# Performance work log

Measured on AMD Instinct MI355X. Metric: run time of the kernel, lower is better.

Reference implementation:

```python
import jax, jax.numpy as jnp
import numpy as np

T, N, DEG = 8, 8192, 15
H = 4


def _gat(x, src, dst, wl, wr, a, b):
    """GATv2Conv with concat=False (heads averaged). x: [N, Cin] -> [N, Cout].
    e_ij = a_h . LeakyReLU(Wl x_j + Wr x_i); softmax over incoming edges of i;
    messages are Wl x_j (PyG GATv2 convention, self-loops already in edge list)."""
    n = x.shape[0]
    h, c = a.shape
    gl = (x @ wl).reshape(n, h, c)  # source-side transform
    gr = (x @ wr).reshape(n, h, c)  # target-side transform
    z = jax.nn.leaky_relu(gl[src] + gr[dst], 0.2)          # [E,H,C]
    e = jnp.einsum('ehc,hc->eh', z, a)                     # [E,H]
    m = jax.ops.segment_max(e, dst, num_segments=n)        # [N,H]
    ex = jnp.exp(e - m[dst])
    den = jax.ops.segment_sum(ex, dst, num_segments=n)     # [N,H]
    msg = jax.ops.segment_sum(ex[:, :, None] * gl[src], dst, num_segments=n)
    return (msg / den[:, :, None]).mean(axis=1) + b


def _d3(x, esrc, edst, wl, wr, a, b):
    # spatio-temporal graph conv: GATv2 applied independently per timestep
    return jax.lax.map(lambda args: _gat(args[0], args[1], args[2], wl, wr, a, b),
                       (x, esrc, edst))


def setup_inputs() -> dict:
    key = jax.random.key(0)
    ks = iter(jax.random.split(key, 32))
    x = jax.random.normal(next(ks), (T, N, 64), dtype=jnp.float32)
    # fixed-degree random graph per timestep + self loops (PyG add_self_loops=True)
    dst_base = jnp.repeat(jnp.arange(N, dtype=jnp.int32), DEG)
    src_r = jax.random.randint(next(ks), (T, N * DEG), 0, N, dtype=jnp.int32)
    loop = jnp.arange(N, dtype=jnp.int32)
    edge_src = jnp.concatenate([src_r, jnp.broadcast_to(loop, (T, N))], axis=1)
    edge_dst = jnp.concatenate([jnp.broadcast_to(dst_base, (T, N * DEG)),
                                jnp.broadcast_to(loop, (T, N))], axis=1)

    def gat_p(k, cin, cout):
        k1, k2, k3 = jax.random.split(k, 3)
        s = 1.0 / np.sqrt(cin)
        return ((jax.random.normal(k1, (cin, H * cout)) * s).astype(jnp.float32),
                (jax.random.normal(k2, (cin, H * cout)) * s).astype(jnp.float32),
                (jax.random.normal(k3, (H, cout)) * s).astype(jnp.float32),
                jnp.zeros((cout,), jnp.float32))

    inp = {"x": x, "edge_src": edge_src, "edge_dst": edge_dst}
    for name, cin, cout in [("c1", 64, 128), ("c2", 128, 64), ("c3", 64, 64), ("c4", 128, 64),
                            ("r11", 64, 64), ("r12", 64, 64), ("r2", 128, 128),
                            ("f11", 64, 64), ("f2", 128, 128)]:
        wl, wr, a, b = gat_p(next(ks), cin, cout)
        inp[name + "_wl"], inp[name + "_wr"], inp[name + "_a"], inp[name + "_b"] = wl, wr, a, b
    # ConvTranspose1d(k=1) == per-node linear conv_ch -> in_channels; then Linear in_channels -> original_dim
    for name, cin, cout in [("r3", 128, 64), ("f3", 128, 64), ("r4", 64, 64), ("f4", 64, 64)]:
        inp[name + "_w"] = (jax.random.normal(next(ks), (cin, cout)) * (1.0 / np.sqrt(cin))).astype(jnp.float32)
        inp[name + "_b"] = jnp.zeros((cout,), jnp.float32)
    return inp


def reference(x, edge_src, edge_dst,
              c1_wl, c1_wr, c1_a, c1_b, c2_wl, c2_wr, c2_a, c2_b,
              c3_wl, c3_wr, c3_a, c3_b, c4_wl, c4_wr, c4_a, c4_b,
              r11_wl, r11_wr, r11_a, r11_b, r12_wl, r12_wr, r12_a, r12_b,
              r2_wl, r2_wr, r2_a, r2_b, r3_w, r3_b, r4_w, r4_b,
              f11_wl, f11_wr, f11_a, f11_b, f2_wl, f2_wr, f2_a, f2_b,
              f3_w, f3_b, f4_w, f4_b):
    elu = jax.nn.elu
    out = elu(_d3(x, edge_src, edge_dst, c1_wl, c1_wr, c1_a, c1_b))           # [T,N,128]
    emb = elu(_d3(out, edge_src, edge_dst, c2_wl, c2_wr, c2_a, c2_b))         # [T,N,64]
    emb = elu(jnp.concatenate([_d3(emb, edge_src, edge_dst, c3_wl, c3_wr, c3_a, c3_b), emb], -1))  # [T,N,128]
    emb = elu(_d3(emb, edge_src, edge_dst, c4_wl, c4_wr, c4_a, c4_b))         # [T,N,64]

    # reconstruction branch on edges at t = -1
    s1, d1 = edge_src[-1], edge_dst[-1]
    r = elu(_gat(emb[-1], s1, d1, r11_wl, r11_wr, r11_a, r11_b))
    r = elu(jnp.concatenate([_gat(r, s1, d1, r12_wl, r12_wr, r12_a, r12_b), r], -1))  # [N,128]
    # F.dropout in eval mode -> identity
    r = elu(_gat(r, s1, d1, r2_wl, r2_wr, r2_a, r2_b))
    r = jnp.tanh(r @ r3_w + r3_b)
    recon = r @ r4_w + r4_b

    # forecasting branch on edges at t = -2 (original reuses reconstruct12 here)
    s2, d2 = edge_src[-2], edge_dst[-2]
    f = elu(_gat(emb[-2], s2, d2, f11_wl, f11_wr, f11_a, f11_b))
    f = elu(jnp.concatenate([_gat(f, s2, d2, r12_wl, r12_wr, r12_a, r12_b), f], -1))
    f = elu(_gat(f, s2, d2, f2_wl, f2_wr, f2_a, f2_b))
    f = jnp.tanh(f @ f3_w + f3_b)
    forecast = f @ f4_w + f4_b
    return (recon, forecast, emb)
```

## Files before the change

### kernel.cpp

```cpp
#include <hip/hip_runtime.h>
#include <cmath>

constexpr int T_   = 8;
constexpr int N_   = 8192;
constexpr int DEG_ = 15;
constexpr int E_   = N_ * (DEG_ + 1);
constexpr float L2E_ = 1.44269504f;

__device__ __forceinline__ float elu1(float v) {
  return v > 0.f ? v : exp2f(v * L2E_) - 1.f;
}

typedef __attribute__((ext_vector_type(8))) short bf16x8;
typedef __attribute__((ext_vector_type(4))) float f32x4;

__device__ __forceinline__ ushort f2bf(float x) {
  uint u = __float_as_uint(x);
  return (ushort)((u + 0x7FFFu + ((u >> 16) & 1u)) >> 16);
}
__device__ __forceinline__ float bf2f(ushort h) {
  return __uint_as_float(((uint)h) << 16);
}

template<int CTRL>
__device__ __forceinline__ float dpp_add(float x) {
  const int t = __builtin_amdgcn_mov_dpp(__float_as_int(x), CTRL, 0xf, 0xf, true);
  return x + __int_as_float(t);
}
__device__ __forceinline__ float row_reduce16(float x) {
  x = dpp_add<0x121>(x);
  x = dpp_add<0x122>(x);
  x = dpp_add<0x124>(x);
  x = dpp_add<0x128>(x);
  return x;
}

__global__ __launch_bounds__(256) void pad_edges(
    const int* __restrict__ es, uint* __restrict__ es16, int total)
{
  const int idx = blockIdx.x * 256 + threadIdx.x;
  if (idx >= total) return;
  const int t = idx >> 13, i = idx & (N_ - 1);
  const int* e = es + (size_t)t * E_ + (size_t)i * DEG_;
  uint o[16];
  #pragma unroll
  for (int k = 0; k < DEG_; k++) o[k] = (uint)e[k];
  o[15] = (uint)i;
  uint4* dst = (uint4*)(es16 + (size_t)idx * 16);
  dst[0] = make_uint4(o[0], o[1], o[2], o[3]);
  dst[1] = make_uint4(o[4], o[5], o[6], o[7]);
  dst[2] = make_uint4(o[8], o[9], o[10], o[11]);
  dst[3] = make_uint4(o[12], o[13], o[14], o[15]);
}

__global__ __launch_bounds__(256) void split_x(
    const float* __restrict__ X, ushort* __restrict__ XH, ushort* __restrict__ XL, int n4)
{
  const int i = blockIdx.x * 256 + threadIdx.x;
  if (i >= n4) return;
  const float4 v = ((const float4*)X)[i];
  const ushort h0 = f2bf(v.x), h1 = f2bf(v.y), h2 = f2bf(v.z), h3 = f2bf(v.w);
  ushort4 hh; hh.x = h0; hh.y = h1; hh.z = h2; hh.w = h3;
  ushort4 ll;
  ll.x = f2bf(v.x - bf2f(h0)); ll.y = f2bf(v.y - bf2f(h1));
  ll.z = f2bf(v.z - bf2f(h2)); ll.w = f2bf(v.w - bf2f(h3));
  ((ushort4*)XH)[i] = hh;
  ((ushort4*)XL)[i] = ll;
}

struct WTable {
  const float* wl[9]; const float* wr[9];
  int lgK[9]; int lgHC[9]; int off[9];
};
__global__ __launch_bounds__(256) void split_wt_all(
    WTable tb, ushort* __restrict__ WH, ushort* __restrict__ WL)
{
  const int y = blockIdx.y;
  const int lgK = tb.lgK[y], lgHC = tb.lgHC[y];
  const int n2 = 2 << (lgK + lgHC);
  const int idx = blockIdx.x * 256 + threadIdx.x;
  if (idx >= n2) return;
  const int k = idx & ((1 << lgK) - 1);
  const int n = (idx >> lgK) & ((1 << lgHC) - 1);
  const int s = idx >> (lgK + lgHC);
  const float* W = s ? tb.wr[y] : tb.wl[y];
  const float v = W[((size_t)k << lgHC) + n];
  const ushort h = f2bf(v);
  WH[tb.off[y] + idx] = h;
  WL[tb.off[y] + idx] = f2bf(v - bf2f(h));
}

__global__ __launch_bounds__(256) void gemm_mfma(
    const ushort* __restrict__ Ah, const ushort* __restrict__ Al,
    const ushort* __restrict__ Wh, const ushort* __restrict__ Wl,
    float* __restrict__ Cl, float* __restrict__ Cr,
    int M, int Ncol, int K, int nt)
{
  __shared__ alignas(16) ushort lAh[4 * 1032];
  __shared__ alignas(16) ushort lAl[4 * 1032];
  __shared__ alignas(16) ushort lBh[4 * 520];
  __shared__ alignas(16) ushort lBl[4 * 520];

  const int z = blockIdx.z;
  const int t = (z < nt) ? z : z - nt;
  const int side = (z < nt) ? 0 : 1;
  const ushort* __restrict__ Bh = Wh + (size_t)side * Ncol * K;
  const ushort* __restrict__ Bl = Wl + (size_t)side * Ncol * K;
  float* __restrict__ C = (side ? Cr : Cl) + (size_t)t * M * Ncol;
  const size_t aoff = (size_t)t * M * K;

  const int bm = blockIdx.x * 128, bn = blockIdx.y * 64;
  const int tid = threadIdx.x;
  const int wid = tid >> 6, lane = tid & 63;
  const int l15 = lane & 15, lk = lane >> 4;

  f32x4 acc[2][4] = {};

  for (int k0 = 0; k0 < K; k0 += 32) {
    #pragma unroll
    for (int c = 0; c < 2; c++) {
      const int ch = tid + c * 256;
      const int row = ch >> 2, kc = ch & 3;
      const size_t ga = aoff + (size_t)(bm + row) * K + (k0 + kc * 8);
      *(uint4*)&lAh[kc * 1032 + row * 8] = *(const uint4*)(Ah + ga);
      *(uint4*)&lAl[kc * 1032 + row * 8] = *(const uint4*)(Al + ga);
    }
    {
      const int col = tid >> 2, kc = tid & 3;
      const size_t gb = (size_t)(bn + col) * K + (k0 + kc * 8);
      *(uint4*)&lBh[kc * 520 + col * 8] = *(const uint4*)(Bh + gb);
      *(uint4*)&lBl[kc * 520 + col * 8] = *(const uint4*)(Bl + gb);
    }
    __syncthreads();

    bf16x8 ah[2], al[2], bh4[4], bl4[4];
    const int r0 = wid * 32;
    #pragma unroll
    for (int rf = 0; rf < 2; rf++) {
      const int ro = (r0 + rf * 16 + l15) * 8;
      ah[rf] = *(const bf16x8*)&lAh[lk * 1032 + ro];
      al[rf] = *(const bf16x8*)&lAl[lk * 1032 + ro];
    }
    #pragma unroll
    for (int cf = 0; cf < 4; cf++) {
      const int co = (cf * 16 + l15) * 8;
      bh4[cf] = *(const bf16x8*)&lBh[lk * 520 + co];
      bl4[cf] = *(const bf16x8*)&lBl[lk * 520 + co];
    }
    #pragma unroll
    for (int rf = 0; rf < 2; rf++)
      #pragma unroll
      for (int cf = 0; cf < 4; cf++) {
        acc[rf][cf] = __builtin_amdgcn_mfma_f32_16x16x32_bf16(ah[rf], bh4[cf], acc[rf][cf], 0, 0, 0);
        acc[rf][cf] = __builtin_amdgcn_mfma_f32_16x16x32_bf16(ah[rf], bl4[cf], acc[rf][cf], 0, 0, 0);
        acc[rf][cf] = __builtin_amdgcn_mfma_f32_16x16x32_bf16(al[rf], bh4[cf], acc[rf][cf], 0, 0, 0);
      }
    __syncthreads();
  }

  #pragma unroll
  for (int rf = 0; rf < 2; rf++)
    #pragma unroll
    for (int cf = 0; cf < 4; cf++) {
      const int col = bn + cf * 16 + l15;
      #pragma unroll
      for (int reg = 0; reg < 4; reg++) {
        const int row = bm + wid * 32 + rf * 16 + lk * 4 + reg;
        C[(size_t)row * Ncol + col] = acc[rf][cf][reg];
      }
    }
}

template<int EPI>
__global__ __launch_bounds__(256) void gemm_k(
    const float* __restrict__ A, const float* __restrict__ B,
    float* __restrict__ C, const float* __restrict__ bias,
    int M, int Ncol, int K)
{
  __shared__ float As[16][68];
  __shared__ float Bs[16][64];

  const int tid = threadIdx.x;
  const int tx = tid & 15, ty = tid >> 4;
  const int bm = blockIdx.x * 64, bn = blockIdx.y * 64;

  const int arow = tid >> 2;
  const int akc  = (tid & 3) * 4;
  const int brow = tid >> 4;
  const int bc4  = (tid & 15) * 4;

  float acc[4][4];
  #pragma unroll
  for (int i = 0; i < 4; i++)
    #pragma unroll
    for (int j = 0; j < 4; j++) acc[i][j] = 0.f;

  for (int k0 = 0; k0 < K; k0 += 16) {
    const float4 va = *(const float4*)(A + (size_t)(bm + arow) * K + (k0 + akc));
    const float4 vb = *(const float4*)(B + (size_t)(k0 + brow) * Ncol + (bn + bc4));
    As[akc + 0][arow] = va.x; As[akc + 1][arow] = va.y;
    As[akc + 2][arow] = va.z; As[akc + 3][arow] = va.w;
    *(float4*)&Bs[brow][bc4] = vb;
    __syncthreads();
    #pragma unroll
    for (int kk = 0; kk < 16; kk++) {
      const float4 av = *(const float4*)&As[kk][ty * 4];
      const float4 bv = *(const float4*)&Bs[kk][tx * 4];
      const float a4[4] = {av.x, av.y, av.z, av.w};
      const float b4[4] = {bv.x, bv.y, bv.z, bv.w};
      #pragma unroll
      for (int i = 0; i < 4; i++)
        #pragma unroll
        for (int j = 0; j < 4; j++)
          acc[i][j] = fmaf(a4[i], b4[j], acc[i][j]);
    }
    __syncthreads();
  }

  #pragma unroll
  for (int i = 0; i < 4; i++) {
    const int row = bm + ty * 4 + i;
    const int col = bn + tx * 4;
    float v[4] = {acc[i][0], acc[i][1], acc[i][2], acc[i][3]};
    #pragma unroll
    for (int j = 0; j < 4; j++) v[j] += bias[col + j];
    if (EPI == 1) {
      #pragma unroll
      for (int j = 0; j < 4; j++) v[j] = tanhf(v[j]);
    }
    *(float4*)(C + (size_t)row * Ncol + col) = make_float4(v[0], v[1], v[2], v[3]);
  }
}

template<bool CONCAT, bool WF32>
__global__ __launch_bounds__(256) void gat_agg256(
    const float* __restrict__ GL, const float* __restrict__ GR,
    const float* __restrict__ aw_, const float* __restrict__ bias,
    const uint* __restrict__ es16, float* __restrict__ out,
    const float* __restrict__ csrc,
    ushort* __restrict__ SHo, ushort* __restrict__ SLo)
{
  constexpr int C = 64;
  constexpr int OSTR = CONCAT ? 128 : 64;

  const int lane = threadIdx.x & 63;
  const int wid  = threadIdx.x >> 6;
  const int t    = blockIdx.x >> 11;
  const int gid  = blockIdx.x * 4 + wid;

  const float* __restrict__ gl = GL + (size_t)t * N_ * 256;
  const uint*  __restrict__ ep = es16 + (size_t)gid * 16;
  const uint lo16 = (uint)lane << 4;

  float gr[4], a6[4], a4c[4];
  {
    const float4 gv = *(const float4*)(GR + (size_t)gid * 256 + lane * 4);
    const float4 av = *(const float4*)(aw_ + lane * 4);
    gr[0] = gv.x; gr[1] = gv.y; gr[2] = gv.z; gr[3] = gv.w;
    a6[0] = 0.6f * L2E_ * av.x; a6[1] = 0.6f * L2E_ * av.y;
    a6[2] = 0.6f * L2E_ * av.z; a6[3] = 0.6f * L2E_ * av.w;
    a4c[0] = 0.4f * L2E_ * av.x; a4c[1] = 0.4f * L2E_ * av.y;
    a4c[2] = 0.4f * L2E_ * av.z; a4c[3] = 0.4f * L2E_ * av.w;
  }

  float acc[4] = {0.f, 0.f, 0.f, 0.f};
  float den = 0.f, m = 0.f;

  #pragma unroll
  for (int b = 0; b < 4; b++) {
    const uint4 j4 = *(const uint4*)(ep + b * 4);
    uint off[4];
    off[0] = (j4.x << 10) + lo16;
    off[1] = (j4.y << 10) + lo16;
    off[2] = (j4.z << 10) + lo16;
    off[3] = (j4.w << 10) + lo16;
    float g[4][4];
    #pragma unroll
    for (int q = 0; q < 4; q++) {
      const float4 v = *(const float4*)((const char*)gl + off[q]);
      g[q][0] = v.x; g[q][1] = v.y; g[q][2] = v.z; g[q][3] = v.w;
    }
    float p[4];
    #pragma unroll
    for (int q = 0; q < 4; q++) {
      float s = 0.f;
      #pragma unroll
      for (int u = 0; u < 4; u++) {
        const float z = g[q][u] + gr[u];
        s = fmaf(z, a6[u], s);
        s = fmaf(fabsf(z), a4c[u], s);
      }
      p[q] = s;
    }
    #pragma unroll
    for (int q = 0; q < 4; q++) p[q] = row_reduce16(p[q]);

    const float bmax = fmaxf(fmaxf(p[0], p[1]), fmaxf(p[2], p[3]));
    if (b == 0) {
      m = bmax;
    } else {
      const float nm = fmaxf(m, bmax);
      const float sc = exp2f(m - nm);
      den *= sc;
      #pragma unroll
      for (int u = 0; u < 4; u++) acc[u] *= sc;
      m = nm;
    }
    #pragma unroll
    for (int q = 0; q < 4; q++) {
      const float w = exp2f(p[q] - m);
      den += w;
      #pragma unroll
      for (int u = 0; u < 4; u++) acc[u] = fmaf(w, g[q][u], acc[u]);
    }
  }

  const float inv = 0.25f / den;
  #pragma unroll
  for (int u = 0; u < 4; u++) acc[u] *= inv;
  #pragma unroll
  for (int u = 0; u < 4; u++) {
    acc[u] += __shfl_xor(acc[u], 16);
    acc[u] += __shfl_xor(acc[u], 32);
  }

  if (lane < 16) {
    float o[4];
    #pragma unroll
    for (int u = 0; u < 4; u++)
      o[u] = elu1(acc[u] + bias[lane * 4 + u]);
    if (WF32)
      *(float4*)(out + (size_t)gid * OSTR + lane * 4) = make_float4(o[0], o[1], o[2], o[3]);
    ushort4 hh, ll;
    hh.x = f2bf(o[0]); hh.y = f2bf(o[1]); hh.z = f2bf(o[2]); hh.w = f2bf(o[3]);
    ll.x = f2bf(o[0] - bf2f(hh.x)); ll.y = f2bf(o[1] - bf2f(hh.y));
    ll.z = f2bf(o[2] - bf2f(hh.z)); ll.w = f2bf(o[3] - bf2f(hh.w));
    *(ushort4*)(SHo + (size_t)gid * OSTR + lane * 4) = hh;
    *(ushort4*)(SLo + (size_t)gid * OSTR + lane * 4) = ll;
  } else if (CONCAT && lane < 32) {
    const int q = lane - 16;
    const float4 v = *(const float4*)(csrc + (size_t)gid * C + q * 4);
    const float o0 = elu1(v.x), o1 = elu1(v.y), o2 = elu1(v.z), o3 = elu1(v.w);
    if (WF32)
      *(float4*)(out + (size_t)gid * OSTR + C + q * 4) = make_float4(o0, o1, o2, o3);
    ushort4 hh, ll;
    hh.x = f2bf(o0); hh.y = f2bf(o1); hh.z = f2bf(o2); hh.w = f2bf(o3);
    ll.x = f2bf(o0 - bf2f(hh.x)); ll.y = f2bf(o1 - bf2f(hh.y));
    ll.z = f2bf(o2 - bf2f(hh.z)); ll.w = f2bf(o3 - bf2f(hh.w));
    *(ushort4*)(SHo + (size_t)gid * OSTR + C + q * 4) = hh;
    *(ushort4*)(SLo + (size_t)gid * OSTR + C + q * 4) = ll;
  }
}

template<bool WF32, bool SPLIT>
__global__ __launch_bounds__(256) void gat_agg512(
    const float* __restrict__ GL, const float* __restrict__ GR,
    const float* __restrict__ aw_, const float* __restrict__ bias,
    const uint* __restrict__ es16, float* __restrict__ out,
    ushort* __restrict__ SHo, ushort* __restrict__ SLo)
{
  const int lane = threadIdx.x & 63;
  const int wid  = threadIdx.x >> 6;
  const int t    = blockIdx.x >> 11;
  const int gid  = blockIdx.x * 4 + wid;

  const float* __restrict__ gl = GL + (size_t)t * N_ * 512;
  const uint*  __restrict__ ep = es16 + (size_t)gid * 16;

  const int s  = lane & 15;
  const int cb = ((lane >> 4) << 7) + (s << 3);
  const uint laneoff = (uint)cb << 2;

  float gr[8], a6[8], a4[8];
  {
    const float4 g0 = *(const float4*)(GR + (size_t)gid * 512 + cb);
    const float4 g1 = *(const float4*)(GR + (size_t)gid * 512 + cb + 4);
    const float4 a0 = *(const float4*)(aw_ + cb);
    const float4 a1 = *(const float4*)(aw_ + cb + 4);
    gr[0] = g0.x; gr[1] = g0.y; gr[2] = g0.z; gr[3] = g0.w;
    gr[4] = g1.x; gr[5] = g1.y; gr[6] = g1.z; gr[7] = g1.w;
    a6[0] = 0.6f * L2E_ * a0.x; a6[1] = 0.6f * L2E_ * a0.y;
    a6[2] = 0.6f * L2E_ * a0.z; a6[3] = 0.6f * L2E_ * a0.w;
    a6[4] = 0.6f * L2E_ * a1.x; a6[5] = 0.6f * L2E_ * a1.y;
    a6[6] = 0.6f * L2E_ * a1.z; a6[7] = 0.6f * L2E_ * a1.w;
    a4[0] = 0.4f * L2E_ * a0.x; a4[1] = 0.4f * L2E_ * a0.y;
    a4[2] = 0.4f * L2E_ * a0.z; a4[3] = 0.4f * L2E_ * a0.w;
    a4[4] = 0.4f * L2E_ * a1.x; a4[5] = 0.4f * L2E_ * a1.y;
    a4[6] = 0.4f * L2E_ * a1.z; a4[7] = 0.4f * L2E_ * a1.w;
  }

  float acc[8] = {0.f, 0.f, 0.f, 0.f, 0.f, 0.f, 0.f, 0.f};
  float den = 0.f, m = 0.f;

  #pragma unroll
  for (int b = 0; b < 4; b++) {
    const uint4 j4 = *(const uint4*)(ep + b * 4);
    uint off[4];
    off[0] = (j4.x << 11) + laneoff;
    off[1] = (j4.y << 11) + laneoff;
    off[2] = (j4.z << 11) + laneoff;
    off[3] = (j4.w << 11) + laneoff;
    float g[4][8];
    #pragma unroll
    for (int q = 0; q < 4; q++) {
      const float4 v0 = *(const float4*)((const char*)gl + off[q]);
      const float4 v1 = *(const float4*)((const char*)gl + off[q] + 16);
      g[q][0] = v0.x; g[q][1] = v0.y; g[q][2] = v0.z; g[q][3] = v0.w;
      g[q][4] = v1.x; g[q][5] = v1.y; g[q][6] = v1.z; g[q][7] = v1.w;
    }
    float p[4];
    #pragma unroll
    for (int q = 0; q < 4; q++) {
      float sc = 0.f;
      #pragma unroll
      for (int u = 0; u < 8; u++) {
        const float z = g[q][u] + gr[u];
        sc = fmaf(z, a6[u], sc);
        sc = fmaf(fabsf(z), a4[u], sc);
      }
      p[q] = sc;
    }
    #pragma unroll
    for (int q = 0; q < 4; q++) p[q] = row_reduce16(p[q]);

    const float bmax = fmaxf(fmaxf(p[0], p[1]), fmaxf(p[2], p[3]));
    if (b == 0) {
      m = bmax;
    } else {
      const float nm = fmaxf(m, bmax);
      const float sc = exp2f(m - nm);
      den *= sc;
      #pragma unroll
      for (int u = 0; u < 8; u++) acc[u] *= sc;
      m = nm;
    }
    #pragma unroll
    for (int q = 0; q < 4; q++) {
      const float w = exp2f(p[q] - m);
      den += w;
      #pragma unroll
      for (int u = 0; u < 8; u++) acc[u] = fmaf(w, g[q][u], acc[u]);
    }
  }

  const float inv = 0.25f / den;
  #pragma unroll
  for (int u = 0; u < 8; u++) acc[u] *= inv;
  #pragma unroll
  for (int u = 0; u < 8; u++) {
    acc[u] += __shfl_xor(acc[u], 16);
    acc[u] += __shfl_xor(acc[u], 32);
  }

  if (lane < 16) {
    float o[8];
    #pragma unroll
    for (int u = 0; u < 8; u++)
      o[u] = elu1(acc[u] + bias[s * 8 + u]);
    if (WF32) {
      *(float4*)(out + (size_t)gid * 128 + s * 8)     = make_float4(o[0], o[1], o[2], o[3]);
      *(float4*)(out + (size_t)gid * 128 + s * 8 + 4) = make_float4(o[4], o[5], o[6], o[7]);
    }
    if (SPLIT) {
      ushort4 h0, h1, l0, l1;
      h0.x = f2bf(o[0]); h0.y = f2bf(o[1]); h0.z = f2bf(o[2]); h0.w = f2bf(o[3]);
      h1.x = f2bf(o[4]); h1.y = f2bf(o[5]); h1.z = f2bf(o[6]); h1.w = f2bf(o[7]);
      l0.x = f2bf(o[0] - bf2f(h0.x)); l0.y = f2bf(o[1] - bf2f(h0.y));
      l0.z = f2bf(o[2] - bf2f(h0.z)); l0.w = f2bf(o[3] - bf2f(h0.w));
      l1.x = f2bf(o[4] - bf2f(h1.x)); l1.y = f2bf(o[5] - bf2f(h1.y));
      l1.z = f2bf(o[6] - bf2f(h1.z)); l1.w = f2bf(o[7] - bf2f(h1.w));
      *(ushort4*)(SHo + (size_t)gid * 128 + s * 8)     = h0;
      *(ushort4*)(SHo + (size_t)gid * 128 + s * 8 + 4) = h1;
      *(ushort4*)(SLo + (size_t)gid * 128 + s * 8)     = l0;
      *(ushort4*)(SLo + (size_t)gid * 128 + s * 8 + 4) = l1;
    }
  }
}

extern "C" void kernel_launch(void* const* d_in, const int* in_sizes, int n_in,
                              void* d_out, int out_size, void* d_ws, size_t ws_size,
                              hipStream_t stream)
{
  (void)in_sizes; (void)n_in; (void)out_size; (void)ws_size;

  const float* x  = (const float*)d_in[0];
  const int*   es = (const int*)d_in[1];
  const float *c1_wl=(const float*)d_in[3], *c1_wr=(const float*)d_in[4], *c1_a=(const float*)d_in[5], *c1_b=(const float*)d_in[6];
  const float *c2_wl=(const float*)d_in[7], *c2_wr=(const float*)d_in[8], *c2_a=(const float*)d_in[9], *c2_b=(const float*)d_in[10];
  const float *c3_wl=(const float*)d_in[11],*c3_wr=(const float*)d_in[12],*c3_a=(const float*)d_in[13],*c3_b=(const float*)d_in[14];
  const float *c4_wl=(const float*)d_in[15],*c4_wr=(const float*)d_in[16],*c4_a=(const float*)d_in[17],*c4_b=(const float*)d_in[18];
  const float *r11_wl=(const float*)d_in[19],*r11_wr=(const float*)d_in[20],*r11_a=(const float*)d_in[21],*r11_b=(const float*)d_in[22];
  const float *r12_wl=(const float*)d_in[23],*r12_wr=(const float*)d_in[24],*r12_a=(const float*)d_in[25],*r12_b=(const float*)d_in[26];
  const float *r2_wl=(const float*)d_in[27],*r2_wr=(const float*)d_in[28],*r2_a=(const float*)d_in[29],*r2_b=(const float*)d_in[30];
  const float *f11_wl=(const float*)d_in[31],*f11_wr=(const float*)d_in[32],*f11_a=(const float*)d_in[33],*f11_b=(const float*)d_in[34];
  const float *f2_wl=(const float*)d_in[35],*f2_wr=(const float*)d_in[36],*f2_a=(const float*)d_in[37],*f2_b=(const float*)d_in[38];
  const float *r3_w=(const float*)d_in[39], *r3_b=(const float*)d_in[40];
  const float *f3_w=(const float*)d_in[41], *f3_b=(const float*)d_in[42];
  const float *r4_w=(const float*)d_in[43], *r4_b=(const float*)d_in[44];
  const float *f4_w=(const float*)d_in[45], *f4_b=(const float*)d_in[46];

  float* ws = (float*)d_ws;
  float* GL = ws;
  float* GR = GL + (size_t)16777216;
  float* A1 = GR + (size_t)16777216;
  float* B0 = A1 + (size_t)T_ * N_ * 64;
  float* B1 = B0 + (size_t)N_ * 128;
  ushort* SH  = (ushort*)(B1 + (size_t)N_ * 128);
  ushort* SL  = SH + (size_t)8388608;
  ushort* SH2 = SL + (size_t)8388608;
  ushort* SL2 = SH2 + (size_t)8388608;
  ushort* WH  = SL2 + (size_t)8388608;
  ushort* WL  = WH + (size_t)589824;
  uint*  ES16 = (uint*)(WL + (size_t)589824);

  float* recon = (float*)d_out;
  float* fcst  = recon + (size_t)N_ * 64;
  float* emb   = fcst + (size_t)N_ * 64;

  const dim3 blk(256);

  pad_edges<<<dim3(T_ * N_ / 256), blk, 0, stream>>>(es, ES16, T_ * N_);
  split_x<<<dim3(T_ * N_ * 64 / 4 / 256), blk, 0, stream>>>(x, SH, SL, T_ * N_ * 64 / 4);
  WTable tb;
  const float* wls[9] = {c1_wl, c2_wl, c3_wl, c4_wl, r11_wl, r12_wl, r2_wl, f11_wl, f2_wl};
  const float* wrs[9] = {c1_wr, c2_wr, c3_wr, c4_wr, r11_wr, r12_wr, r2_wr, f11_wr, f2_wr};
  const int Ks[9]  = {64, 128, 64, 128, 64, 64, 128, 64, 128};
  const int HCs[9] = {512, 256, 256, 256, 256, 256, 512, 256, 512};
  int woff[9]; int acc_off = 0;
  for (int y = 0; y < 9; y++) {
    tb.wl[y] = wls[y]; tb.wr[y] = wrs[y];
    tb.lgK[y] = __builtin_ctz(Ks[y]); tb.lgHC[y] = __builtin_ctz(HCs[y]);
    woff[y] = acc_off; tb.off[y] = acc_off;
    acc_off += 2 * Ks[y] * HCs[y];
  }
  split_wt_all<<<dim3(512, 9), blk, 0, stream>>>(tb, WH, WL);

  for (int ch = 0; ch < 2; ch++) {
    const int t0 = ch * 4, nt = 4;
    gemm_mfma<<<dim3(N_ / 128, 8, 2 * nt), blk, 0, stream>>>(
        SH + (size_t)t0 * N_ * 64, SL + (size_t)t0 * N_ * 64,
        WH + woff[0], WL + woff[0], GL, GR, N_, 512, 64, nt);
    gat_agg512<false, true><<<dim3(nt * N_ / 4), blk, 0, stream>>>(
        GL, GR, c1_a, c1_b, ES16 + (size_t)t0 * N_ * 16, nullptr,
        SH2 + (size_t)t0 * N_ * 128, SL2 + (size_t)t0 * N_ * 128);
  }
  gemm_mfma<<<dim3(N_ / 128, 4, 2 * T_), blk, 0, stream>>>(
      SH2, SL2, WH + woff[1], WL + woff[1], GL, GR, N_, 256, 128, T_);
  gat_agg256<false, true><<<dim3(T_ * N_ / 4), blk, 0, stream>>>(
      GL, GR, c2_a, c2_b, ES16, A1, nullptr, SH, SL);
  gemm_mfma<<<dim3(N_ / 128, 4, 2 * T_), blk, 0, stream>>>(
      SH, SL, WH + woff[2], WL + woff[2], GL, GR, N_, 256, 64, T_);
  gat_agg256<true, false><<<dim3(T_ * N_ / 4), blk, 0, stream>>>(
      GL, GR, c3_a, c3_b, ES16, nullptr, A1, SH, SL);
  gemm_mfma<<<dim3(N_ / 128, 4, 2 * T_), blk, 0, stream>>>(
      SH, SL, WH + woff[3], WL + woff[3], GL, GR, N_, 256, 128, T_);
  gat_agg256<false, true><<<dim3(T_ * N_ / 4), blk, 0, stream>>>(
      GL, GR, c4_a, c4_b, ES16, emb, nullptr, SH2, SL2);

  const uint* esR = ES16 + (size_t)7 * N_ * 16;
  gemm_mfma<<<dim3(N_ / 128, 4, 2), blk, 0, stream>>>(
      SH2 + (size_t)7 * N_ * 64, SL2 + (size_t)7 * N_ * 64,
      WH + woff[4], WL + woff[4], GL, GR, N_, 256, 64, 1);
  gat_agg256<false, true><<<dim3(N_ / 4), blk, 0, stream>>>(
      GL, GR, r11_a, r11_b, esR, B0, nullptr, SH, SL);
  gemm_mfma<<<dim3(N_ / 128, 4, 2), blk, 0, stream>>>(
      SH, SL, WH + woff[5], WL + woff[5], GL, GR, N_, 256, 64, 1);
  gat_agg256<true, false><<<dim3(N_ / 4), blk, 0, stream>>>(
      GL, GR, r12_a, r12_b, esR, nullptr, B0, SH, SL);
  gemm_mfma<<<dim3(N_ / 128, 8, 2), blk, 0, stream>>>(
      SH, SL, WH + woff[6], WL + woff[6], GL, GR, N_, 512, 128, 1);
  gat_agg512<true, false><<<dim3(N_ / 4), blk, 0, stream>>>(
      GL, GR, r2_a, r2_b, esR, B0, nullptr, nullptr);
  gemm_k<1><<<dim3(N_ / 64, 1, 1), blk, 0, stream>>>(B0, r3_w, B1, r3_b, N_, 64, 128);
  gemm_k<2><<<dim3(N_ / 64, 1, 1), blk, 0, stream>>>(B1, r4_w, recon, r4_b, N_, 64, 64);

  const uint* esF = ES16 + (size_t)6 * N_ * 16;
  gemm_mfma<<<dim3(N_ / 128, 4, 2), blk, 0, stream>>>(
      SH2 + (size_t)6 * N_ * 64, SL2 + (size_t)6 * N_ * 64,
      WH + woff[7], WL + woff[7], GL, GR, N_, 256, 64, 1);
  gat_agg256<false, true><<<dim3(N_ / 4), blk, 0, stream>>>(
      GL, GR, f11_a, f11_b, esF, B0, nullptr, SH, SL);
  gemm_mfma<<<dim3(N_ / 128, 4, 2), blk, 0, stream>>>(
      SH, SL, WH + woff[5], WL + woff[5], GL, GR, N_, 256, 64, 1);
  gat_agg256<true, false><<<dim3(N_ / 4), blk, 0, stream>>>(
      GL, GR, r12_a, r12_b, esF, nullptr, B0, SH, SL);
  gemm_mfma<<<dim3(N_ / 128, 8, 2), blk, 0, stream>>>(
      SH, SL, WH + woff[8], WL + woff[8], GL, GR, N_, 512, 128, 1);
  gat_agg512<true, false><<<dim3(N_ / 4), blk, 0, stream>>>(
      GL, GR, f2_a, f2_b, esF, B0, nullptr, nullptr);
  gemm_k<1><<<dim3(N_ / 64, 1, 1), blk, 0, stream>>>(B0, f3_w, B1, f3_b, N_, 64, 128);
  gemm_k<2><<<dim3(N_ / 64, 1, 1), blk, 0, stream>>>(B1, f4_w, fcst, f4_b, N_, 64, 64);
}
```

Before: 1.001 ms.

## Swizzle GAT aggregation blocks by XCD and give each wave one head in agg512

Block indices in the aggregation kernels are remapped so that blocks landing on the same XCD work on the same timestep. The aim is to keep each XCD's gathered source-feature rows in its own L2 instead of spreading every timestep over all XCDs. gat_agg512 is also restructured to process one node per block, with each of the 4 waves handling one head over 2 channels per lane. The heads are then summed through shared memory after a block barrier. This trades a fourfold larger grid and a __syncthreads for smaller per-lane register arrays and narrower, more coalesced loads.

```diff
diff --git a/kernel.cpp b/kernel.cpp
--- a/kernel.cpp
+++ b/kernel.cpp
@@ -232,7 +232,7 @@
   }
 }
 
-template<bool CONCAT, bool WF32>
+template<bool SWZ, bool CONCAT, bool WF32>
 __global__ __launch_bounds__(256) void gat_agg256(
     const float* __restrict__ GL, const float* __restrict__ GR,
     const float* __restrict__ aw_, const float* __restrict__ bias,
@@ -245,8 +245,10 @@
 
   const int lane = threadIdx.x & 63;
   const int wid  = threadIdx.x >> 6;
-  const int t    = blockIdx.x >> 11;
-  const int gid  = blockIdx.x * 4 + wid;
+  const int bid  = blockIdx.x;
+  const int t    = SWZ ? (bid & 7) : 0;
+  const int ib   = SWZ ? (bid >> 3) : bid;
+  const int gid  = t * N_ + ib * 4 + wid;
 
   const float* __restrict__ gl = GL + (size_t)t * N_ * 256;
   const uint*  __restrict__ ep = es16 + (size_t)gid * 16;
@@ -352,127 +354,112 @@
   }
 }
 
-template<bool WF32, bool SPLIT>
+template<bool SWZ, bool WF32, bool SPLIT>
 __global__ __launch_bounds__(256) void gat_agg512(
     const float* __restrict__ GL, const float* __restrict__ GR,
     const float* __restrict__ aw_, const float* __restrict__ bias,
     const uint* __restrict__ es16, float* __restrict__ out,
     ushort* __restrict__ SHo, ushort* __restrict__ SLo)
 {
+  __shared__ float smem[4][128];
+
   const int lane = threadIdx.x & 63;
-  const int wid  = threadIdx.x >> 6;
-  const int t    = blockIdx.x >> 11;
-  const int gid  = blockIdx.x * 4 + wid;
+  const int h    = threadIdx.x >> 6;
+  const int bid  = blockIdx.x;
+  int t, i;
+  if (SWZ) {
+    const int xcd = bid & 7;
+    t = xcd >> 1;
+    i = ((bid >> 3) << 1) | (xcd & 1);
+  } else {
+    t = 0; i = bid;
+  }
+  const int gid = t * N_ + i;
 
   const float* __restrict__ gl = GL + (size_t)t * N_ * 512;
   const uint*  __restrict__ ep = es16 + (size_t)gid * 16;
-
-  const int s  = lane & 15;
-  const int cb = ((lane >> 4) << 7) + (s << 3);
-  const uint laneoff = (uint)cb << 2;
-
-  float gr[8], a6[8], a4[8];
+  const int cb = h * 128 + lane * 2;
+  const uint cbo = (uint)cb << 2;
+
+  float gr0, gr1, a60, a61, a40, a41;
   {
-    const float4 g0 = *(const float4*)(GR + (size_t)gid * 512 + cb);
-    const float4 g1 = *(const float4*)(GR + (size_t)gid * 512 + cb + 4);
-    const float4 a0 = *(const float4*)(aw_ + cb);
-    const float4 a1 = *(const float4*)(aw_ + cb + 4);
-    gr[0] = g0.x; gr[1] = g0.y; gr[2] = g0.z; gr[3] = g0.w;
-    gr[4] = g1.x; gr[5] = g1.y; gr[6] = g1.z; gr[7] = g1.w;
-    a6[0] = 0.6f * L2E_ * a0.x; a6[1] = 0.6f * L2E_ * a0.y;
-    a6[2] = 0.6f * L2E_ * a0.z; a6[3] = 0.6f * L2E_ * a0.w;
-    a6[4] = 0.6f * L2E_ * a1.x; a6[5] = 0.6f * L2E_ * a1.y;
-    a6[6] = 0.6f * L2E_ * a1.z; a6[7] = 0.6f * L2E_ * a1.w;
-    a4[0] = 0.4f * L2E_ * a0.x; a4[1] = 0.4f * L2E_ * a0.y;
-    a4[2] = 0.4f * L2E_ * a0.z; a4[3] = 0.4f * L2E_ * a0.w;
-    a4[4] = 0.4f * L2E_ * a1.x; a4[5] = 0.4f * L2E_ * a1.y;
-    a4[6] = 0.4f * L2E_ * a1.z; a4[7] = 0.4f * L2E_ * a1.w;
-  }
-
-  float acc[8] = {0.f, 0.f, 0.f, 0.f, 0.f, 0.f, 0.f, 0.f};
-  float den = 0.f, m = 0.f;
+    const float2 gv = *(const float2*)(GR + (size_t)gid * 512 + cb);
+    const float2 av = *(const float2*)(aw_ + cb);
+    gr0 = gv.x; gr1 = gv.y;
+    a60 = 0.6f * L2E_ * av.x; a61 = 0.6f * L2E_ * av.y;
+    a40 = 0.4f * L2E_ * av.x; a41 = 0.4f * L2E_ * av.y;
+  }
+
+  float acc0 = 0.f, acc1 = 0.f, den = 0.f, m = 0.f;
 
   #pragma unroll
   for (int b = 0; b < 4; b++) {
     const uint4 j4 = *(const uint4*)(ep + b * 4);
     uint off[4];
-    off[0] = (j4.x << 11) + laneoff;
-    off[1] = (j4.y << 11) + laneoff;
-    off[2] = (j4.z << 11) + laneoff;
-    off[3] = (j4.w << 11) + laneoff;
-    float g[4][8];
-    #pragma unroll
-    for (int q = 0; q < 4; q++) {
-      const float4 v0 = *(const float4*)((const char*)gl + off[q]);
-      const float4 v1 = *(const float4*)((const char*)gl + off[q] + 16);
-      g[q][0] = v0.x; g[q][1] = v0.y; g[q][2] = v0.z; g[q][3] = v0.w;
-      g[q][4] = v1.x; g[q][5] = v1.y; g[q][6] = v1.z; g[q][7] = v1.w;
+    off[0] = (j4.x << 11) + cbo;
+    off[1] = (j4.y << 11) + cbo;
+    off[2] = (j4.z << 11) + cbo;
+    off[3] = (j4.w << 11) + cbo;
+    float g[4][2];
+    #pragma unroll
+    for (int q = 0; q < 4; q++) {
+      const float2 v = *(const float2*)((const char*)gl + off[q]);
+      g[q][0] = v.x; g[q][1] = v.y;
     }
     float p[4];
     #pragma unroll
     for (int q = 0; q < 4; q++) {
-      float sc = 0.f;
-      #pragma unroll
-      for (int u = 0; u < 8; u++) {
-        const float z = g[q][u] + gr[u];
-        sc = fmaf(z, a6[u], sc);
-        sc = fmaf(fabsf(z), a4[u], sc);
-      }
-      p[q] = sc;
-    }
-    #pragma unroll
-    for (int q = 0; q < 4; q++) p[q] = row_reduce16(p[q]);
-
+      const float z0 = g[q][0] + gr0;
+      const float z1 = g[q][1] + gr1;
+      float s = z0 * a60;
+      s = fmaf(fabsf(z0), a40, s);
+      s = fmaf(z1, a61, s);
+      s = fmaf(fabsf(z1), a41, s);
+      p[q] = s;
+    }
+    #pragma unroll
+    for (int q = 0; q < 4; q++) {
+      p[q] = row_reduce16(p[q]);
+      p[q] += __shfl_xor(p[q], 16);
+      p[q] += __shfl_xor(p[q], 32);
+    }
     const float bmax = fmaxf(fmaxf(p[0], p[1]), fmaxf(p[2], p[3]));
     if (b == 0) {
       m = bmax;
     } else {
       const float nm = fmaxf(m, bmax);
       const float sc = exp2f(m - nm);
-      den *= sc;
-      #pragma unroll
-      for (int u = 0; u < 8; u++) acc[u] *= sc;
+      den *= sc; acc0 *= sc; acc1 *= sc;
       m = nm;
     }
     #pragma unroll
     for (int q = 0; q < 4; q++) {
       const float w = exp2f(p[q] - m);
       den += w;
-      #pragma unroll
-      for (int u = 0; u < 8; u++) acc[u] = fmaf(w, g[q][u], acc[u]);
+      acc0 = fmaf(w, g[q][0], acc0);
+      acc1 = fmaf(w, g[q][1], acc1);
     }
   }
 
   const float inv = 0.25f / den;
-  #pragma unroll
-  for (int u = 0; u < 8; u++) acc[u] *= inv;
-  #pragma unroll
-  for (int u = 0; u < 8; u++) {
-    acc[u] += __shfl_xor(acc[u], 16);
-    acc[u] += __shfl_xor(acc[u], 32);
-  }
-
-  if (lane < 16) {
-    float o[8];
-    #pragma unroll
-    for (int u = 0; u < 8; u++)
-      o[u] = elu1(acc[u] + bias[s * 8 + u]);
-    if (WF32) {
-      *(float4*)(out + (size_t)gid * 128 + s * 8)     = make_float4(o[0], o[1], o[2], o[3]);
-      *(float4*)(out + (size_t)gid * 128 + s * 8 + 4) = make_float4(o[4], o[5], o[6], o[7]);
-    }
+  smem[h][lane * 2]     = acc0 * inv;
+  smem[h][lane * 2 + 1] = acc1 * inv;
+  __syncthreads();
+
+  if (h == 0) {
+    const int c = lane * 2;
+    float s0 = smem[0][c] + smem[1][c] + smem[2][c] + smem[3][c];
+    float s1 = smem[0][c + 1] + smem[1][c + 1] + smem[2][c + 1] + smem[3][c + 1];
+    s0 = elu1(s0 + bias[c]);
+    s1 = elu1(s1 + bias[c + 1]);
+    if (WF32)
+      *(float2*)(out + (size_t)gid * 128 + c) = make_float2(s0, s1);
     if (SPLIT) {
-      ushort4 h0, h1, l0, l1;
-      h0.x = f2bf(o[0]); h0.y = f2bf(o[1]); h0.z = f2bf(o[2]); h0.w = f2bf(o[3]);
-      h1.x = f2bf(o[4]); h1.y = f2bf(o[5]); h1.z = f2bf(o[6]); h1.w = f2bf(o[7]);
-      l0.x = f2bf(o[0] - bf2f(h0.x)); l0.y = f2bf(o[1] - bf2f(h0.y));
-      l0.z = f2bf(o[2] - bf2f(h0.z)); l0.w = f2bf(o[3] - bf2f(h0.w));
-      l1.x = f2bf(o[4] - bf2f(h1.x)); l1.y = f2bf(o[5] - bf2f(h1.y));
-      l1.z = f2bf(o[6] - bf2f(h1.z)); l1.w = f2bf(o[7] - bf2f(h1.w));
-      *(ushort4*)(SHo + (size_t)gid * 128 + s * 8)     = h0;
-      *(ushort4*)(SHo + (size_t)gid * 128 + s * 8 + 4) = h1;
-      *(ushort4*)(SLo + (size_t)gid * 128 + s * 8)     = l0;
-      *(ushort4*)(SLo + (size_t)gid * 128 + s * 8 + 4) = l1;
+      ushort2 hh, ll;
+      hh.x = f2bf(s0); hh.y = f2bf(s1);
+      ll.x = f2bf(s0 - bf2f(hh.x)); ll.y = f2bf(s1 - bf2f(hh.y));
+      *(ushort2*)(SHo + (size_t)gid * 128 + c) = hh;
+      *(ushort2*)(SLo + (size_t)gid * 128 + c) = ll;
     }
   }
 }
@@ -540,36 +527,36 @@
     gemm_mfma<<<dim3(N_ / 128, 8, 2 * nt), blk, 0, stream>>>(
         SH + (size_t)t0 * N_ * 64, SL + (size_t)t0 * N_ * 64,
         WH + woff[0], WL + woff[0], GL, GR, N_, 512, 64, nt);
-    gat_agg512<false, true><<<dim3(nt * N_ / 4), blk, 0, stream>>>(
+    gat_agg512<true, false, true><<<dim3(nt * N_), blk, 0, stream>>>(
         GL, GR, c1_a, c1_b, ES16 + (size_t)t0 * N_ * 16, nullptr,
         SH2 + (size_t)t0 * N_ * 128, SL2 + (size_t)t0 * N_ * 128);
   }
   gemm_mfma<<<dim3(N_ / 128, 4, 2 * T_), blk, 0, stream>>>(
       SH2, SL2, WH + woff[1], WL + woff[1], GL, GR, N_, 256, 128, T_);
-  gat_agg256<false, true><<<dim3(T_ * N_ / 4), blk, 0, stream>>>(
+  gat_agg256<true, false, true><<<dim3(T_ * N_ / 4), blk, 0, stream>>>(
       GL, GR, c2_a, c2_b, ES16, A1, nullptr, SH, SL);
   gemm_mfma<<<dim3(N_ / 128, 4, 2 * T_), blk, 0, stream>>>(
       SH, SL, WH + woff[2], WL + woff[2], GL, GR, N_, 256, 64, T_);
-  gat_agg256<true, false><<<dim3(T_ * N_ / 4), blk, 0, stream>>>(
+  gat_agg256<true, true, false><<<dim3(T_ * N_ / 4), blk, 0, stream>>>(
       GL, GR, c3_a, c3_b, ES16, nullptr, A1, SH, SL);
   gemm_mfma<<<dim3(N_ / 128, 4, 2 * T_), blk, 0, stream>>>(
       SH, SL, WH + woff[3], WL + woff[3], GL, GR, N_, 256, 128, T_);
-  gat_agg256<false, true><<<dim3(T_ * N_ / 4), blk, 0, stream>>>(
+  gat_agg256<true, false, true><<<dim3(T_ * N_ / 4), blk, 0, stream>>>(
       GL, GR, c4_a, c4_b, ES16, emb, nullptr, SH2, SL2);
 
   const uint* esR = ES16 + (size_t)7 * N_ * 16;
   gemm_mfma<<<dim3(N_ / 128, 4, 2), blk, 0, stream>>>(
       SH2 + (size_t)7 * N_ * 64, SL2 + (size_t)7 * N_ * 64,
       WH + woff[4], WL + woff[4], GL, GR, N_, 256, 64, 1);
-  gat_agg256<false, true><<<dim3(N_ / 4), blk, 0, stream>>>(
+  gat_agg256<false, false, true><<<dim3(N_ / 4), blk, 0, stream>>>(
       GL, GR, r11_a, r11_b, esR, B0, nullptr, SH, SL);
   gemm_mfma<<<dim3(N_ / 128, 4, 2), blk, 0, stream>>>(
       SH, SL, WH + woff[5], WL + woff[5], GL, GR, N_, 256, 64, 1);
-  gat_agg256<true, false><<<dim3(N_ / 4), blk, 0, stream>>>(
+  gat_agg256<false, true, false><<<dim3(N_ / 4), blk, 0, stream>>>(
       GL, GR, r12_a, r12_b, esR, nullptr, B0, SH, SL);
   gemm_mfma<<<dim3(N_ / 128, 8, 2), blk, 0, stream>>>(
       SH, SL, WH + woff[6], WL + woff[6], GL, GR, N_, 512, 128, 1);
-  gat_agg512<true, false><<<dim3(N_ / 4), blk, 0, stream>>>(
+  gat_agg512<false, true, false><<<dim3(N_), blk, 0, stream>>>(
       GL, GR, r2_a, r2_b, esR, B0, nullptr, nullptr);
   gemm_k<1><<<dim3(N_ / 64, 1, 1), blk, 0, stream>>>(B0, r3_w, B1, r3_b, N_, 64, 128);
   gemm_k<2><<<dim3(N_ / 64, 1, 1), blk, 0, stream>>>(B1, r4_w, recon, r4_b, N_, 64, 64);
@@ -578,15 +565,15 @@
   gemm_mfma<<<dim3(N_ / 128, 4, 2), blk, 0, stream>>>(
       SH2 + (size_t)6 * N_ * 64, SL2 + (size_t)6 * N_ * 64,
       WH + woff[7], WL + woff[7], GL, GR, N_, 256, 64, 1);
-  gat_agg256<false, true><<<dim3(N_ / 4), blk, 0, stream>>>(
+  gat_agg256<false, false, true><<<dim3(N_ / 4), blk, 0, stream>>>(
       GL, GR, f11_a, f11_b, esF, B0, nullptr, SH, SL);
   gemm_mfma<<<dim3(N_ / 128, 4, 2), blk, 0, stream>>>(
       SH, SL, WH + woff[5], WL + woff[5], GL, GR, N_, 256, 64, 1);
-  gat_agg256<true, false><<<dim3(N_ / 4), blk, 0, stream>>>(
+  gat_agg256<false, true, false><<<dim3(N_ / 4), blk, 0, stream>>>(
       GL, GR, r12_a, r12_b, esF, nullptr, B0, SH, SL);
   gemm_mfma<<<dim3(N_ / 128, 8, 2), blk, 0, stream>>>(
       SH, SL, WH + woff[8], WL + woff[8], GL, GR, N_, 512, 128, 1);
-  gat_agg512<true, false><<<dim3(N_ / 4), blk, 0, stream>>>(
+  gat_agg512<false, true, false><<<dim3(N_), blk, 0, stream>>>(
       GL, GR, f2_a, f2_b, esF, B0, nullptr, nullptr);
   gemm_k<1><<<dim3(N_ / 64, 1, 1), blk, 0, stream>>>(B0, f3_w, B1, f3_b, N_, 64, 128);
   gemm_k<2><<<dim3(N_ / 64, 1, 1), blk, 0, stream>>>(B1, f4_w, fcst, f4_b, N_, 64, 64);
```

After: 957.1 us. 1.05x faster.
